# Performance work log

Measured on AMD Instinct MI355X. Metric: run time of the kernel, lower is better.

Reference implementation:

```python
import jax, jax.numpy as jnp
import numpy as np

N_NODES = 100000
N_EDGES = 1600000
N_FEAT = 128
HIDDEN = 16
EMBED = 128
N_GRAPHS = 64


def setup_inputs() -> dict:
    key = jax.random.key(0)
    ks = jax.random.split(key, 6)
    x = jax.random.normal(ks[0], (N_NODES, N_FEAT), dtype=jnp.float32)
    edge_index = jax.random.randint(ks[1], (2, N_EDGES), 0, N_NODES, dtype=jnp.int32)
    batch = jnp.sort(jax.random.randint(ks[2], (N_NODES,), 0, N_GRAPHS, dtype=jnp.int32))
    W1 = jax.random.normal(ks[3], (N_FEAT, HIDDEN), dtype=jnp.float32) * (1.0 / np.sqrt(N_FEAT))
    b1 = jnp.zeros((HIDDEN,), dtype=jnp.float32)
    W2 = jax.random.normal(ks[4], (HIDDEN, EMBED), dtype=jnp.float32) * (1.0 / np.sqrt(HIDDEN))
    b2 = jnp.zeros((EMBED,), dtype=jnp.float32)
    return {"x": x, "edge_index": edge_index, "batch": batch,
            "W1": W1, "b1": b1, "W2": W2, "b2": b2}


def _gcn_conv(x, W, b, src, dst, dinv):
    # x' = D^{-1/2} (A + I) D^{-1/2} (x W) + b ; (src, dst) already include self-loops
    h = x @ W                                   # [N, out]
    norm = dinv[src] * dinv[dst]                # [E']
    msg = h[src] * norm[:, None]                # gather + scale
    out = jax.ops.segment_sum(msg, dst, num_segments=x.shape[0])  # scatter-add
    return out + b


def reference(x, edge_index, batch, W1, b1, W2, b2):
    n = x.shape[0]
    loop = jnp.arange(n, dtype=edge_index.dtype)
    src = jnp.concatenate([edge_index[0], loop])  # add self-loops
    dst = jnp.concatenate([edge_index[1], loop])
    deg = jax.ops.segment_sum(jnp.ones_like(dst, dtype=x.dtype), dst, num_segments=n)
    dinv = jnp.where(deg > 0, jax.lax.rsqrt(deg), 0.0)

    h = _gcn_conv(x, W1, b1, src, dst, dinv)
    h = jax.nn.relu(h)
    # dropout(p=0.2) is identity in eval mode
    h = _gcn_conv(h, W2, b2, src, dst, dinv)

    # mean pooling over graphs in the batch
    sums = jax.ops.segment_sum(h, batch, num_segments=N_GRAPHS)          # [G, EMBED]
    cnt = jax.ops.segment_sum(jnp.ones((n,), dtype=h.dtype), batch, num_segments=N_GRAPHS)
    return sums / jnp.maximum(cnt, 1.0)[:, None]
```

## Files before the change

### kernel.cpp

```cpp
#include <hip/hip_runtime.h>

#define HIDDEN 16
#define N_FEAT 128
#define EMBED 128
#define N_GRAPHS 64
#define BSH 8
#define MAXB 512

__global__ void k_hist(const int* __restrict__ dst, int n_edges, int nbuck,
                       int* __restrict__ ghist) {
    __shared__ int h[MAXB];
    for (int i = threadIdx.x; i < MAXB; i += blockDim.x) h[i] = 0;
    __syncthreads();
    int base = blockIdx.x * blockDim.x * 4;
    for (int j = 0; j < 4; j++) {
        int e = base + j * blockDim.x + threadIdx.x;
        if (e < n_edges) atomicAdd(&h[dst[e] >> BSH], 1);
    }
    __syncthreads();
    for (int b = threadIdx.x; b < nbuck; b += blockDim.x)
        if (h[b]) atomicAdd(&ghist[b], h[b]);
}

__global__ void k_scan(const int* __restrict__ ghist, int nbuck,
                       int* __restrict__ gbase, int* __restrict__ gfill) {
    __shared__ int s[MAXB];
    int t = threadIdx.x;
    s[t] = (t < nbuck) ? ghist[t] : 0;
    __syncthreads();
    for (int st = 1; st < MAXB; st <<= 1) {
        int v = (t >= st) ? s[t - st] : 0;
        __syncthreads();
        s[t] += v;
        __syncthreads();
    }
    if (t < nbuck) {
        int excl = s[t] - ghist[t];
        gbase[t] = excl;
        gfill[t] = excl;
    }
}

__global__ void __launch_bounds__(1024)
k_part(const int* __restrict__ src, const int* __restrict__ dst,
       int n_edges, int nbuck, int* __restrict__ gfill, uint2* __restrict__ ebuf) {
    __shared__ int hcnt[MAXB];
    __shared__ int hexcl[MAXB];
    __shared__ int hrank[MAXB];
    __shared__ int hbase[MAXB];
    __shared__ uint2 stage[4096];
    int tid = threadIdx.x;
    for (int i = tid; i < MAXB; i += 1024) { hcnt[i] = 0; hrank[i] = 0; }
    __syncthreads();
    int base = blockIdx.x * 4096;
    int cnt = min(4096, n_edges - base);
    int s_[4], d_[4];
#pragma unroll
    for (int j = 0; j < 4; j++) {
        int k = j * 1024 + tid;
        if (k < cnt) {
            s_[j] = src[base + k]; d_[j] = dst[base + k];
            atomicAdd(&hcnt[d_[j] >> BSH], 1);
        }
    }
    __syncthreads();
    if (tid < MAXB) hexcl[tid] = hcnt[tid];
    __syncthreads();
    for (int st = 1; st < MAXB; st <<= 1) {
        int v = 0;
        if (tid < MAXB && tid >= st) v = hexcl[tid - st];
        __syncthreads();
        if (tid < MAXB) hexcl[tid] += v;
        __syncthreads();
    }
    if (tid < nbuck && hcnt[tid] > 0)
        hbase[tid] = atomicAdd(&gfill[tid], hcnt[tid]);
    __syncthreads();
#pragma unroll
    for (int j = 0; j < 4; j++) {
        int k = j * 1024 + tid;
        if (k < cnt) {
            int b = d_[j] >> BSH;
            int r = atomicAdd(&hrank[b], 1);
            stage[hexcl[b] - hcnt[b] + r] = make_uint2((unsigned)s_[j], (unsigned)d_[j]);
        }
    }
    __syncthreads();
    for (int t = tid; t < cnt; t += 1024) {
        uint2 e = stage[t];
        int b = (int)(e.y >> BSH);
        ebuf[hbase[b] + (t - (hexcl[b] - hcnt[b]))] = e;
    }
}

__global__ void __launch_bounds__(1024)
k_csr(const uint2* __restrict__ ebuf, const int* __restrict__ gbase,
      const int* __restrict__ ghist, int n,
      int* __restrict__ deg, int* __restrict__ rowp, int* __restrict__ col) {
    __shared__ int nh[256], nexcl[256], nrank[256];
    int b = blockIdx.x;
    int tid = threadIdx.x;
    int seg0 = gbase[b];
    int cnt = ghist[b];
    int nb0 = b << BSH;
    if (tid < 256) { nh[tid] = 0; nrank[tid] = 0; }
    __syncthreads();
    for (int t = tid; t < cnt; t += 1024)
        atomicAdd(&nh[ebuf[seg0 + t].y - nb0], 1);
    __syncthreads();
    if (tid < 256) nexcl[tid] = nh[tid];
    __syncthreads();
    for (int st = 1; st < 256; st <<= 1) {
        int v = 0;
        if (tid < 256 && tid >= st) v = nexcl[tid - st];
        __syncthreads();
        if (tid < 256) nexcl[tid] += v;
        __syncthreads();
    }
    if (tid < 256) {
        int node = nb0 + tid;
        if (node < n) {
            deg[node]  = nh[tid];
            rowp[node] = seg0 + nexcl[tid] - nh[tid];
        }
    }
    __syncthreads();
    for (int t = tid; t < cnt; t += 1024) {
        uint2 e = ebuf[seg0 + t];
        int ln = (int)e.y - nb0;
        int r = atomicAdd(&nrank[ln], 1);
        col[seg0 + (nexcl[ln] - nh[ln]) + r] = (int)e.x;
    }
}

__global__ void k_gemm1(const float* __restrict__ x, const float* __restrict__ W1,
                        const int* __restrict__ deg, float* __restrict__ dinv,
                        float* __restrict__ Hs, int n) {
    __shared__ float Ws[N_FEAT * HIDDEN];
    int tid = threadIdx.x;
    {
        const float4* w4 = (const float4*)W1;
        float4* s4 = (float4*)Ws;
        s4[tid * 2]     = w4[tid * 2];
        s4[tid * 2 + 1] = w4[tid * 2 + 1];
    }
    __syncthreads();
    int i = blockIdx.x * blockDim.x + tid;
    if (i >= n) return;

    float acc[HIDDEN];
#pragma unroll
    for (int o = 0; o < HIDDEN; o++) acc[o] = 0.f;

    const float4* xr = (const float4*)(x + (size_t)i * N_FEAT);
#pragma unroll 8
    for (int k4 = 0; k4 < N_FEAT / 4; k4++) {
        float4 xv = xr[k4];
        const float* w0 = &Ws[(k4 * 4 + 0) * HIDDEN];
        const float* w1 = &Ws[(k4 * 4 + 1) * HIDDEN];
        const float* w2 = &Ws[(k4 * 4 + 2) * HIDDEN];
        const float* w3 = &Ws[(k4 * 4 + 3) * HIDDEN];
#pragma unroll
        for (int o = 0; o < HIDDEN; o++)
            acc[o] += xv.x * w0[o] + xv.y * w1[o] + xv.z * w2[o] + xv.w * w3[o];
    }
    float di = rsqrtf((float)deg[i] + 1.0f);
    dinv[i] = di;
    float4* hout = (float4*)(Hs + (size_t)i * HIDDEN);
#pragma unroll
    for (int q = 0; q < 4; q++) {
        float4 v;
        v.x = acc[q * 4 + 0] * di; v.y = acc[q * 4 + 1] * di;
        v.z = acc[q * 4 + 2] * di; v.w = acc[q * 4 + 3] * di;
        hout[q] = v;
    }
}

template <int LAYER>
__global__ void k_pull(const float* __restrict__ V, const int* __restrict__ rowptr,
                       const int* __restrict__ deg, const int* __restrict__ col,
                       const float* __restrict__ dinv, const float* __restrict__ b1,
                       float* __restrict__ out, int n) {
    int wid = (blockIdx.x * blockDim.x + threadIdx.x) >> 6;
    int lane = threadIdx.x & 63;
    if (wid >= n) return;
    int f  = lane & 15;
    int es = lane >> 4;
    int start = rowptr[wid];
    int dg = deg[wid];
    float acc = 0.f;
    for (int j = es; j < dg; j += 4) {
        int s = col[start + j];
        acc += V[(size_t)s * HIDDEN + f];
    }
    acc += __shfl_xor(acc, 16, 64);
    acc += __shfl_xor(acc, 32, 64);
    if (lane < 16) {
        float tot = acc + V[(size_t)wid * HIDDEN + f];
        float di = dinv[wid];
        float r;
        if (LAYER == 1) r = fmaxf(di * tot + b1[f], 0.f) * di;
        else            r = di * tot;
        out[(size_t)wid * HIDDEN + f] = r;
    }
}

__global__ void k_pool(const float* __restrict__ R, const int* __restrict__ batch,
                       float* __restrict__ S, float* __restrict__ cnt, int n) {
    __shared__ float ls[8][HIDDEN];
    __shared__ float lc[8];
    int tid = threadIdx.x;
    if (tid < 8) lc[tid] = 0.f;
    if (tid < 8 * HIDDEN) ((float*)ls)[tid] = 0.f;
    __syncthreads();

    int i0 = blockIdx.x * blockDim.x;
    int g0 = batch[i0 < n ? i0 : (n - 1)];
    int i = i0 + tid;
    if (i < n) {
        int g = batch[i];
        const float* r = R + (size_t)i * HIDDEN;
        int off = g - g0;
        if (off >= 0 && off < 8) {
#pragma unroll
            for (int o = 0; o < HIDDEN; o++) atomicAdd(&ls[off][o], r[o]);
            atomicAdd(&lc[off], 1.f);
        } else {
#pragma unroll
            for (int o = 0; o < HIDDEN; o++) atomicAdd(&S[(size_t)g * HIDDEN + o], r[o]);
            atomicAdd(&cnt[g], 1.f);
        }
    }
    __syncthreads();
    if (tid < 8 * HIDDEN) {
        int bb = tid >> 4, o = tid & 15;
        int g = g0 + bb;
        float v = ls[bb][o];
        if (v != 0.f && g < N_GRAPHS) atomicAdd(&S[(size_t)g * HIDDEN + o], v);
    }
    if (tid < 8) {
        int g = g0 + tid;
        float c = lc[tid];
        if (c != 0.f && g < N_GRAPHS) atomicAdd(&cnt[g], c);
    }
}

__global__ void k_out(const float* __restrict__ S, const float* __restrict__ cnt,
                      const float* __restrict__ W2, const float* __restrict__ b2,
                      float* __restrict__ out) {
    int g = blockIdx.x;
    int e = threadIdx.x;
    float c = cnt[g];
    float acc = 0.f;
#pragma unroll
    for (int k = 0; k < HIDDEN; k++) acc += S[g * HIDDEN + k] * W2[k * EMBED + e];
    out[g * EMBED + e] = (c > 0.f) ? (acc / c + b2[e]) : 0.f;
}

extern "C" void kernel_launch(void* const* d_in, const int* in_sizes, int n_in,
                              void* d_out, int out_size, void* d_ws, size_t ws_size,
                              hipStream_t stream) {
    const float* x     = (const float*)d_in[0];
    const int*   ei    = (const int*)  d_in[1];
    const int*   batch = (const int*)  d_in[2];
    const float* W1    = (const float*)d_in[3];
    const float* b1    = (const float*)d_in[4];
    const float* W2    = (const float*)d_in[5];
    const float* b2    = (const float*)d_in[6];
    float* out = (float*)d_out;

    const int n       = in_sizes[2];
    const int n_edges = in_sizes[1] / 2;
    const int* srcp = ei;
    const int* dstp = ei + n_edges;
    const int nbuck = (n + 255) >> BSH;

    float* ws    = (float*)d_ws;
    float* Hs    = ws;
    float* Q     = Hs + (size_t)n * HIDDEN;
    float* dinv  = Q + (size_t)n * HIDDEN;
    int*   deg   = (int*)(dinv + n);
    int*   rowp  = deg + n;
    int*   col   = rowp + n;
    int*   ghist = col + n_edges;
    int*   gbase = ghist + MAXB;
    int*   gfill = gbase + MAXB;
    float* S     = (float*)(gfill + MAXB);
    float* cnt   = S + N_GRAPHS * HIDDEN;
    uint2* ebuf  = (uint2*)Hs;

    hipMemsetAsync(ghist, 0, MAXB * sizeof(int), stream);
    hipMemsetAsync(S, 0, (N_GRAPHS * HIDDEN + N_GRAPHS) * sizeof(float), stream);

    const int pb4k = (n_edges + 4095) / 4096;
    k_hist<<<pb4k, 1024, 0, stream>>>(dstp, n_edges, nbuck, ghist);
    k_scan<<<1, MAXB, 0, stream>>>(ghist, nbuck, gbase, gfill);
    k_part<<<pb4k, 1024, 0, stream>>>(srcp, dstp, n_edges, nbuck, gfill, ebuf);
    k_csr <<<nbuck, 1024, 0, stream>>>(ebuf, gbase, ghist, n, deg, rowp, col);

    const int nb = (n + 255) / 256;
    k_gemm1<<<nb, 256, 0, stream>>>(x, W1, deg, dinv, Hs, n);

    const int pullb = (n * 64 + 255) / 256;
    k_pull<1><<<pullb, 256, 0, stream>>>(Hs, rowp, deg, col, dinv, b1, Q, n);
    k_pull<2><<<pullb, 256, 0, stream>>>(Q,  rowp, deg, col, dinv, b1, Hs, n);

    k_pool<<<nb, 256, 0, stream>>>(Hs, batch, S, cnt, n);
    k_out <<<N_GRAPHS, EMBED, 0, stream>>>(S, cnt, W2, b2, out);
}
```

Baseline: 279.0 us.

## Replace CSR build with bucketed aggregation, bf16 features, fused layer-2 pooling

Drops the per-node CSR construction and instead aggregates directly over the destination-bucketed edge buffer, packing the source index and local destination into a single 32-bit word. Hidden features are stored as bf16 pairs to halve gather traffic. The second-layer aggregation is fused with mean pooling, so edge messages are accumulated straight into per-graph sums without materialising layer-2 node outputs. This trades the CSR column build and one full node-feature pass for shared-memory atomics and reduced precision. The 8-bit local-index packing also assumes source indices fit in 24 bits.

```diff
diff --git a/kernel.cpp b/kernel.cpp
--- a/kernel.cpp
+++ b/kernel.cpp
@@ -7,18 +7,31 @@
 #define BSH 8
 #define MAXB 512
 
-__global__ void k_hist(const int* __restrict__ dst, int n_edges, int nbuck,
-                       int* __restrict__ ghist) {
+typedef unsigned int uint;
+
+__device__ inline uint pk2(float a, float b) {
+    uint ua = __float_as_uint(a), ub = __float_as_uint(b);
+    ua = (ua + 0x7FFFu + ((ua >> 16) & 1u)) >> 16;
+    ub = (ub + 0x7FFFu + ((ub >> 16) & 1u)) & 0xFFFF0000u;
+    return ua | ub;
+}
+__device__ inline float2 upk2(uint w) {
+    return make_float2(__uint_as_float(w << 16), __uint_as_float(w & 0xFFFF0000u));
+}
+
+__global__ void __launch_bounds__(1024)
+k_hist(const int* __restrict__ dst, int n_edges, int nbuck, int* __restrict__ ghist) {
     __shared__ int h[MAXB];
-    for (int i = threadIdx.x; i < MAXB; i += blockDim.x) h[i] = 0;
-    __syncthreads();
-    int base = blockIdx.x * blockDim.x * 4;
+    for (int i = threadIdx.x; i < MAXB; i += 1024) h[i] = 0;
+    __syncthreads();
+    int base = blockIdx.x * 4096;
+#pragma unroll
     for (int j = 0; j < 4; j++) {
-        int e = base + j * blockDim.x + threadIdx.x;
+        int e = base + j * 1024 + threadIdx.x;
         if (e < n_edges) atomicAdd(&h[dst[e] >> BSH], 1);
     }
     __syncthreads();
-    for (int b = threadIdx.x; b < nbuck; b += blockDim.x)
+    for (int b = threadIdx.x; b < nbuck; b += 1024)
         if (h[b]) atomicAdd(&ghist[b], h[b]);
 }
 
@@ -43,7 +56,7 @@
 
 __global__ void __launch_bounds__(1024)
 k_part(const int* __restrict__ src, const int* __restrict__ dst,
-       int n_edges, int nbuck, int* __restrict__ gfill, uint2* __restrict__ ebuf) {
+       int n_edges, int nbuck, int* __restrict__ gfill, uint* __restrict__ ebuf) {
     __shared__ int hcnt[MAXB];
     __shared__ int hexcl[MAXB];
     __shared__ int hrank[MAXB];
@@ -82,60 +95,35 @@
         if (k < cnt) {
             int b = d_[j] >> BSH;
             int r = atomicAdd(&hrank[b], 1);
-            stage[hexcl[b] - hcnt[b] + r] = make_uint2((unsigned)s_[j], (unsigned)d_[j]);
+            stage[hexcl[b] - hcnt[b] + r] = make_uint2((uint)s_[j], (uint)d_[j]);
         }
     }
     __syncthreads();
     for (int t = tid; t < cnt; t += 1024) {
         uint2 e = stage[t];
         int b = (int)(e.y >> BSH);
-        ebuf[hbase[b] + (t - (hexcl[b] - hcnt[b]))] = e;
-    }
-}
-
-__global__ void __launch_bounds__(1024)
-k_csr(const uint2* __restrict__ ebuf, const int* __restrict__ gbase,
-      const int* __restrict__ ghist, int n,
-      int* __restrict__ deg, int* __restrict__ rowp, int* __restrict__ col) {
-    __shared__ int nh[256], nexcl[256], nrank[256];
-    int b = blockIdx.x;
-    int tid = threadIdx.x;
-    int seg0 = gbase[b];
-    int cnt = ghist[b];
-    int nb0 = b << BSH;
-    if (tid < 256) { nh[tid] = 0; nrank[tid] = 0; }
-    __syncthreads();
+        ebuf[hbase[b] + (t - (hexcl[b] - hcnt[b]))] = (e.x << 8) | (e.y & 255u);
+    }
+}
+
+__global__ void __launch_bounds__(1024)
+k_deg2(const uint* __restrict__ ebuf, const int* __restrict__ gbase,
+       const int* __restrict__ ghist, int n, int* __restrict__ deg) {
+    __shared__ int nh[256];
+    int tid = threadIdx.x;
+    if (tid < 256) nh[tid] = 0;
+    __syncthreads();
+    int seg0 = gbase[blockIdx.x], cnt = ghist[blockIdx.x];
     for (int t = tid; t < cnt; t += 1024)
-        atomicAdd(&nh[ebuf[seg0 + t].y - nb0], 1);
-    __syncthreads();
-    if (tid < 256) nexcl[tid] = nh[tid];
-    __syncthreads();
-    for (int st = 1; st < 256; st <<= 1) {
-        int v = 0;
-        if (tid < 256 && tid >= st) v = nexcl[tid - st];
-        __syncthreads();
-        if (tid < 256) nexcl[tid] += v;
-        __syncthreads();
-    }
-    if (tid < 256) {
-        int node = nb0 + tid;
-        if (node < n) {
-            deg[node]  = nh[tid];
-            rowp[node] = seg0 + nexcl[tid] - nh[tid];
-        }
-    }
-    __syncthreads();
-    for (int t = tid; t < cnt; t += 1024) {
-        uint2 e = ebuf[seg0 + t];
-        int ln = (int)e.y - nb0;
-        int r = atomicAdd(&nrank[ln], 1);
-        col[seg0 + (nexcl[ln] - nh[ln]) + r] = (int)e.x;
-    }
+        atomicAdd(&nh[ebuf[seg0 + t] & 255u], 1);
+    __syncthreads();
+    int node = (blockIdx.x << BSH) + tid;
+    if (tid < 256 && node < n) deg[node] = nh[tid];
 }
 
 __global__ void k_gemm1(const float* __restrict__ x, const float* __restrict__ W1,
                         const int* __restrict__ deg, float* __restrict__ dinv,
-                        float* __restrict__ Hs, int n) {
+                        uint* __restrict__ Hs2, int n) {
     __shared__ float Ws[N_FEAT * HIDDEN];
     int tid = threadIdx.x;
     {
@@ -166,64 +154,83 @@
     }
     float di = rsqrtf((float)deg[i] + 1.0f);
     dinv[i] = di;
-    float4* hout = (float4*)(Hs + (size_t)i * HIDDEN);
-#pragma unroll
-    for (int q = 0; q < 4; q++) {
-        float4 v;
-        v.x = acc[q * 4 + 0] * di; v.y = acc[q * 4 + 1] * di;
-        v.z = acc[q * 4 + 2] * di; v.w = acc[q * 4 + 3] * di;
-        hout[q] = v;
-    }
-}
-
-template <int LAYER>
-__global__ void k_pull(const float* __restrict__ V, const int* __restrict__ rowptr,
-                       const int* __restrict__ deg, const int* __restrict__ col,
-                       const float* __restrict__ dinv, const float* __restrict__ b1,
-                       float* __restrict__ out, int n) {
-    int wid = (blockIdx.x * blockDim.x + threadIdx.x) >> 6;
-    int lane = threadIdx.x & 63;
-    if (wid >= n) return;
-    int f  = lane & 15;
-    int es = lane >> 4;
-    int start = rowptr[wid];
-    int dg = deg[wid];
-    float acc = 0.f;
-    for (int j = es; j < dg; j += 4) {
-        int s = col[start + j];
-        acc += V[(size_t)s * HIDDEN + f];
-    }
-    acc += __shfl_xor(acc, 16, 64);
-    acc += __shfl_xor(acc, 32, 64);
-    if (lane < 16) {
-        float tot = acc + V[(size_t)wid * HIDDEN + f];
-        float di = dinv[wid];
-        float r;
-        if (LAYER == 1) r = fmaxf(di * tot + b1[f], 0.f) * di;
-        else            r = di * tot;
-        out[(size_t)wid * HIDDEN + f] = r;
-    }
-}
-
-__global__ void k_pool(const float* __restrict__ R, const int* __restrict__ batch,
-                       float* __restrict__ S, float* __restrict__ cnt, int n) {
-    __shared__ float ls[8][HIDDEN];
+    uint o8[8];
+#pragma unroll
+    for (int j = 0; j < 8; j++) o8[j] = pk2(acc[2 * j] * di, acc[2 * j + 1] * di);
+    uint4* hp = (uint4*)(Hs2 + (size_t)i * 8);
+    hp[0] = make_uint4(o8[0], o8[1], o8[2], o8[3]);
+    hp[1] = make_uint4(o8[4], o8[5], o8[6], o8[7]);
+}
+
+__global__ void __launch_bounds__(1024)
+k_agg1(const uint* __restrict__ ebuf, const int* __restrict__ gbase,
+       const int* __restrict__ ghist, const uint* __restrict__ Hs2,
+       const float* __restrict__ dinv, const float* __restrict__ b1,
+       uint* __restrict__ Q2, int n) {
+    __shared__ float Qa[256 * 17];
+    __shared__ float b1s[HIDDEN];
+    int tid = threadIdx.x;
+    for (int i = tid; i < 256 * 17; i += 1024) Qa[i] = 0.f;
+    if (tid < HIDDEN) b1s[tid] = b1[tid];
+    __syncthreads();
+    int seg0 = gbase[blockIdx.x], cnt = ghist[blockIdx.x];
+    int gid = tid >> 3, fp = tid & 7;
+    for (int t = gid; t < cnt; t += 128) {
+        uint e = ebuf[seg0 + t];
+        int s = (int)(e >> 8), ln = (int)(e & 255u);
+        float2 v = upk2(Hs2[(size_t)s * 8 + fp]);
+        atomicAdd(&Qa[ln * 17 + 2 * fp],     v.x);
+        atomicAdd(&Qa[ln * 17 + 2 * fp + 1], v.y);
+    }
+    __syncthreads();
+    int node = (blockIdx.x << BSH) + tid;
+    if (tid < 256 && node < n) {
+        float di = dinv[node];
+        float q[HIDDEN];
+#pragma unroll
+        for (int j = 0; j < 8; j++) {
+            float2 h = upk2(Hs2[(size_t)node * 8 + j]);
+            q[2 * j]     = Qa[tid * 17 + 2 * j]     + h.x;
+            q[2 * j + 1] = Qa[tid * 17 + 2 * j + 1] + h.y;
+        }
+        uint o8[8];
+#pragma unroll
+        for (int j = 0; j < 8; j++) {
+            float a = fmaxf(di * q[2 * j]     + b1s[2 * j],     0.f) * di;
+            float b = fmaxf(di * q[2 * j + 1] + b1s[2 * j + 1], 0.f) * di;
+            o8[j] = pk2(a, b);
+        }
+        uint4* qp = (uint4*)(Q2 + (size_t)node * 8);
+        qp[0] = make_uint4(o8[0], o8[1], o8[2], o8[3]);
+        qp[1] = make_uint4(o8[4], o8[5], o8[6], o8[7]);
+    }
+}
+
+__global__ void k_selfpool(const uint* __restrict__ Q2, const int* __restrict__ batch,
+                           const float* __restrict__ dinv,
+                           float* __restrict__ S, float* __restrict__ cnt, int n) {
+    __shared__ float ls[8 * HIDDEN];
     __shared__ float lc[8];
     int tid = threadIdx.x;
     if (tid < 8) lc[tid] = 0.f;
-    if (tid < 8 * HIDDEN) ((float*)ls)[tid] = 0.f;
-    __syncthreads();
-
-    int i0 = blockIdx.x * blockDim.x;
+    if (tid < 8 * HIDDEN) ls[tid] = 0.f;
+    __syncthreads();
+    int i0 = blockIdx.x * 256;
     int g0 = batch[i0 < n ? i0 : (n - 1)];
     int i = i0 + tid;
     if (i < n) {
         int g = batch[i];
-        const float* r = R + (size_t)i * HIDDEN;
+        float di = dinv[i];
+        float r[HIDDEN];
+#pragma unroll
+        for (int j = 0; j < 8; j++) {
+            float2 v = upk2(Q2[(size_t)i * 8 + j]);
+            r[2 * j] = di * v.x; r[2 * j + 1] = di * v.y;
+        }
         int off = g - g0;
         if (off >= 0 && off < 8) {
 #pragma unroll
-            for (int o = 0; o < HIDDEN; o++) atomicAdd(&ls[off][o], r[o]);
+            for (int o = 0; o < HIDDEN; o++) atomicAdd(&ls[off * HIDDEN + o], r[o]);
             atomicAdd(&lc[off], 1.f);
         } else {
 #pragma unroll
@@ -233,9 +240,9 @@
     }
     __syncthreads();
     if (tid < 8 * HIDDEN) {
-        int bb = tid >> 4, o = tid & 15;
-        int g = g0 + bb;
-        float v = ls[bb][o];
+        int b = tid >> 4, o = tid & 15;
+        int g = g0 + b;
+        float v = ls[b * HIDDEN + o];
         if (v != 0.f && g < N_GRAPHS) atomicAdd(&S[(size_t)g * HIDDEN + o], v);
     }
     if (tid < 8) {
@@ -243,6 +250,50 @@
         float c = lc[tid];
         if (c != 0.f && g < N_GRAPHS) atomicAdd(&cnt[g], c);
     }
+}
+
+__global__ void __launch_bounds__(1024)
+k_edge2(const uint* __restrict__ ebuf, const int* __restrict__ gbase,
+        const int* __restrict__ ghist, const uint* __restrict__ Q2,
+        const int* __restrict__ batch, const float* __restrict__ dinv,
+        float* __restrict__ S, int n) {
+    __shared__ float Sl[N_GRAPHS * HIDDEN];
+    __shared__ int   batL[256];
+    __shared__ float dinvL[256];
+    int tid = threadIdx.x;
+    Sl[tid] = 0.f;
+    if (tid < 256) {
+        int node = (blockIdx.x << BSH) + tid;
+        batL[tid]  = (node < n) ? batch[node] : 0;
+        dinvL[tid] = (node < n) ? dinv[node]  : 0.f;
+    }
+    __syncthreads();
+    int seg0 = gbase[blockIdx.x], cnt = ghist[blockIdx.x];
+    int gid = tid >> 3, fp = tid & 7;
+    int gc = -1;
+    float ax = 0.f, ay = 0.f;
+    for (int t = gid; t < cnt; t += 128) {
+        uint e = ebuf[seg0 + t];
+        int s = (int)(e >> 8), ln = (int)(e & 255u);
+        int g = batL[ln];
+        if (g != gc) {
+            if (gc >= 0) {
+                atomicAdd(&Sl[gc * HIDDEN + 2 * fp],     ax);
+                atomicAdd(&Sl[gc * HIDDEN + 2 * fp + 1], ay);
+            }
+            gc = g; ax = 0.f; ay = 0.f;
+        }
+        float di = dinvL[ln];
+        float2 v = upk2(Q2[(size_t)s * 8 + fp]);
+        ax += di * v.x; ay += di * v.y;
+    }
+    if (gc >= 0) {
+        atomicAdd(&Sl[gc * HIDDEN + 2 * fp],     ax);
+        atomicAdd(&Sl[gc * HIDDEN + 2 * fp + 1], ay);
+    }
+    __syncthreads();
+    float v = Sl[tid];
+    if (v != 0.f) atomicAdd(&S[tid], v);
 }
 
 __global__ void k_out(const float* __restrict__ S, const float* __restrict__ cnt,
@@ -275,36 +326,30 @@
     const int* dstp = ei + n_edges;
     const int nbuck = (n + 255) >> BSH;
 
-    float* ws    = (float*)d_ws;
-    float* Hs    = ws;
-    float* Q     = Hs + (size_t)n * HIDDEN;
-    float* dinv  = Q + (size_t)n * HIDDEN;
+    uint*  Hs2   = (uint*)d_ws;
+    uint*  Q2    = Hs2 + (size_t)n * 8;
+    float* dinv  = (float*)(Q2 + (size_t)n * 8);
     int*   deg   = (int*)(dinv + n);
-    int*   rowp  = deg + n;
-    int*   col   = rowp + n;
-    int*   ghist = col + n_edges;
+    uint*  ebuf  = (uint*)(deg + n);
+    int*   ghist = (int*)(ebuf + n_edges);
     int*   gbase = ghist + MAXB;
     int*   gfill = gbase + MAXB;
     float* S     = (float*)(gfill + MAXB);
     float* cnt   = S + N_GRAPHS * HIDDEN;
-    uint2* ebuf  = (uint2*)Hs;
 
     hipMemsetAsync(ghist, 0, MAXB * sizeof(int), stream);
     hipMemsetAsync(S, 0, (N_GRAPHS * HIDDEN + N_GRAPHS) * sizeof(float), stream);
 
     const int pb4k = (n_edges + 4095) / 4096;
-    k_hist<<<pb4k, 1024, 0, stream>>>(dstp, n_edges, nbuck, ghist);
-    k_scan<<<1, MAXB, 0, stream>>>(ghist, nbuck, gbase, gfill);
-    k_part<<<pb4k, 1024, 0, stream>>>(srcp, dstp, n_edges, nbuck, gfill, ebuf);
-    k_csr <<<nbuck, 1024, 0, stream>>>(ebuf, gbase, ghist, n, deg, rowp, col);
+    k_hist <<<pb4k, 1024, 0, stream>>>(dstp, n_edges, nbuck, ghist);
+    k_scan <<<1, MAXB, 0, stream>>>(ghist, nbuck, gbase, gfill);
+    k_part <<<pb4k, 1024, 0, stream>>>(srcp, dstp, n_edges, nbuck, gfill, ebuf);
+    k_deg2 <<<nbuck, 1024, 0, stream>>>(ebuf, gbase, ghist, n, deg);
 
     const int nb = (n + 255) / 256;
-    k_gemm1<<<nb, 256, 0, stream>>>(x, W1, deg, dinv, Hs, n);
-
-    const int pullb = (n * 64 + 255) / 256;
-    k_pull<1><<<pullb, 256, 0, stream>>>(Hs, rowp, deg, col, dinv, b1, Q, n);
-    k_pull<2><<<pullb, 256, 0, stream>>>(Q,  rowp, deg, col, dinv, b1, Hs, n);
-
-    k_pool<<<nb, 256, 0, stream>>>(Hs, batch, S, cnt, n);
-    k_out <<<N_GRAPHS, EMBED, 0, stream>>>(S, cnt, W2, b2, out);
-}
+    k_gemm1<<<nb, 256, 0, stream>>>(x, W1, deg, dinv, Hs2, n);
+    k_agg1 <<<nbuck, 1024, 0, stream>>>(ebuf, gbase, ghist, Hs2, dinv, b1, Q2, n);
+    k_selfpool<<<nb, 256, 0, stream>>>(Q2, batch, dinv, S, cnt, n);
+    k_edge2<<<nbuck, 1024, 0, stream>>>(ebuf, gbase, ghist, Q2, batch, dinv, S, n);
+    k_out  <<<N_GRAPHS, EMBED, 0, stream>>>(S, cnt, W2, b2, out);
+}
```

New measurement: 425.3 us. 1.52x slower.

## Store node features as bf16 pairs and pack edges into single words

Applied to the files above, without the earlier changes.

Node features Hs and Q are now stored as packed bf16 pairs, which halves the bytes read in the random gathers of both pull kernels. Each wavefront now spreads 8 edges across 8 lanes per feature pair. Edges in the partition buffer are packed as (src<<8 | dst&255), halving partition traffic, and the bucket index is recovered by a binary search over the shared-memory prefix sums. The cost is bf16 rounding error in the intermediate features, plus a log-time search per staged edge.

```diff
diff --git a/kernel.cpp b/kernel.cpp
--- a/kernel.cpp
+++ b/kernel.cpp
@@ -7,18 +7,31 @@
 #define BSH 8
 #define MAXB 512
 
-__global__ void k_hist(const int* __restrict__ dst, int n_edges, int nbuck,
-                       int* __restrict__ ghist) {
+typedef unsigned int uint;
+
+__device__ inline uint pk2(float a, float b) {
+    uint ua = __float_as_uint(a), ub = __float_as_uint(b);
+    ua = (ua + 0x7FFFu + ((ua >> 16) & 1u)) >> 16;
+    ub = (ub + 0x7FFFu + ((ub >> 16) & 1u)) & 0xFFFF0000u;
+    return ua | ub;
+}
+__device__ inline float2 upk2(uint w) {
+    return make_float2(__uint_as_float(w << 16), __uint_as_float(w & 0xFFFF0000u));
+}
+
+__global__ void __launch_bounds__(1024)
+k_hist(const int* __restrict__ dst, int n_edges, int nbuck, int* __restrict__ ghist) {
     __shared__ int h[MAXB];
-    for (int i = threadIdx.x; i < MAXB; i += blockDim.x) h[i] = 0;
-    __syncthreads();
-    int base = blockIdx.x * blockDim.x * 4;
+    for (int i = threadIdx.x; i < MAXB; i += 1024) h[i] = 0;
+    __syncthreads();
+    int base = blockIdx.x * 4096;
+#pragma unroll
     for (int j = 0; j < 4; j++) {
-        int e = base + j * blockDim.x + threadIdx.x;
+        int e = base + j * 1024 + threadIdx.x;
         if (e < n_edges) atomicAdd(&h[dst[e] >> BSH], 1);
     }
     __syncthreads();
-    for (int b = threadIdx.x; b < nbuck; b += blockDim.x)
+    for (int b = threadIdx.x; b < nbuck; b += 1024)
         if (h[b]) atomicAdd(&ghist[b], h[b]);
 }
 
@@ -43,12 +56,12 @@
 
 __global__ void __launch_bounds__(1024)
 k_part(const int* __restrict__ src, const int* __restrict__ dst,
-       int n_edges, int nbuck, int* __restrict__ gfill, uint2* __restrict__ ebuf) {
+       int n_edges, int nbuck, int* __restrict__ gfill, uint* __restrict__ ebuf) {
     __shared__ int hcnt[MAXB];
     __shared__ int hexcl[MAXB];
     __shared__ int hrank[MAXB];
     __shared__ int hbase[MAXB];
-    __shared__ uint2 stage[4096];
+    __shared__ uint stage[4096];
     int tid = threadIdx.x;
     for (int i = tid; i < MAXB; i += 1024) { hcnt[i] = 0; hrank[i] = 0; }
     __syncthreads();
@@ -82,19 +95,24 @@
         if (k < cnt) {
             int b = d_[j] >> BSH;
             int r = atomicAdd(&hrank[b], 1);
-            stage[hexcl[b] - hcnt[b] + r] = make_uint2((unsigned)s_[j], (unsigned)d_[j]);
+            stage[hexcl[b] - hcnt[b] + r] = ((uint)s_[j] << 8) | ((uint)d_[j] & 255u);
         }
     }
     __syncthreads();
     for (int t = tid; t < cnt; t += 1024) {
-        uint2 e = stage[t];
-        int b = (int)(e.y >> BSH);
+        uint e = stage[t];
+        int lo = 0, hi = MAXB - 1;
+        while (lo < hi) {
+            int mid = (lo + hi) >> 1;
+            if (t < hexcl[mid]) hi = mid; else lo = mid + 1;
+        }
+        int b = lo;
         ebuf[hbase[b] + (t - (hexcl[b] - hcnt[b]))] = e;
     }
 }
 
 __global__ void __launch_bounds__(1024)
-k_csr(const uint2* __restrict__ ebuf, const int* __restrict__ gbase,
+k_csr(const uint* __restrict__ ebuf, const int* __restrict__ gbase,
       const int* __restrict__ ghist, int n,
       int* __restrict__ deg, int* __restrict__ rowp, int* __restrict__ col) {
     __shared__ int nh[256], nexcl[256], nrank[256];
@@ -106,7 +124,7 @@
     if (tid < 256) { nh[tid] = 0; nrank[tid] = 0; }
     __syncthreads();
     for (int t = tid; t < cnt; t += 1024)
-        atomicAdd(&nh[ebuf[seg0 + t].y - nb0], 1);
+        atomicAdd(&nh[ebuf[seg0 + t] & 255u], 1);
     __syncthreads();
     if (tid < 256) nexcl[tid] = nh[tid];
     __syncthreads();
@@ -126,16 +144,16 @@
     }
     __syncthreads();
     for (int t = tid; t < cnt; t += 1024) {
-        uint2 e = ebuf[seg0 + t];
-        int ln = (int)e.y - nb0;
+        uint e = ebuf[seg0 + t];
+        int ln = (int)(e & 255u);
         int r = atomicAdd(&nrank[ln], 1);
-        col[seg0 + (nexcl[ln] - nh[ln]) + r] = (int)e.x;
+        col[seg0 + (nexcl[ln] - nh[ln]) + r] = (int)(e >> 8);
     }
 }
 
 __global__ void k_gemm1(const float* __restrict__ x, const float* __restrict__ W1,
                         const int* __restrict__ deg, float* __restrict__ dinv,
-                        float* __restrict__ Hs, int n) {
+                        uint* __restrict__ Hs2, int n) {
     __shared__ float Ws[N_FEAT * HIDDEN];
     int tid = threadIdx.x;
     {
@@ -166,55 +184,59 @@
     }
     float di = rsqrtf((float)deg[i] + 1.0f);
     dinv[i] = di;
-    float4* hout = (float4*)(Hs + (size_t)i * HIDDEN);
-#pragma unroll
-    for (int q = 0; q < 4; q++) {
-        float4 v;
-        v.x = acc[q * 4 + 0] * di; v.y = acc[q * 4 + 1] * di;
-        v.z = acc[q * 4 + 2] * di; v.w = acc[q * 4 + 3] * di;
-        hout[q] = v;
-    }
+    uint o8[8];
+#pragma unroll
+    for (int j = 0; j < 8; j++) o8[j] = pk2(acc[2 * j] * di, acc[2 * j + 1] * di);
+    uint4* hp = (uint4*)(Hs2 + (size_t)i * 8);
+    hp[0] = make_uint4(o8[0], o8[1], o8[2], o8[3]);
+    hp[1] = make_uint4(o8[4], o8[5], o8[6], o8[7]);
 }
 
 template <int LAYER>
-__global__ void k_pull(const float* __restrict__ V, const int* __restrict__ rowptr,
+__global__ void k_pull(const uint* __restrict__ V2, const int* __restrict__ rowptr,
                        const int* __restrict__ deg, const int* __restrict__ col,
                        const float* __restrict__ dinv, const float* __restrict__ b1,
-                       float* __restrict__ out, int n) {
+                       uint* __restrict__ Q2, float2* __restrict__ R2, int n) {
     int wid = (blockIdx.x * blockDim.x + threadIdx.x) >> 6;
     int lane = threadIdx.x & 63;
     if (wid >= n) return;
-    int f  = lane & 15;
-    int es = lane >> 4;
+    int f  = lane & 7;
+    int es = lane >> 3;
     int start = rowptr[wid];
     int dg = deg[wid];
-    float acc = 0.f;
-    for (int j = es; j < dg; j += 4) {
+    float ax = 0.f, ay = 0.f;
+    for (int j = es; j < dg; j += 8) {
         int s = col[start + j];
-        acc += V[(size_t)s * HIDDEN + f];
-    }
-    acc += __shfl_xor(acc, 16, 64);
-    acc += __shfl_xor(acc, 32, 64);
-    if (lane < 16) {
-        float tot = acc + V[(size_t)wid * HIDDEN + f];
+        float2 v = upk2(V2[(size_t)s * 8 + f]);
+        ax += v.x; ay += v.y;
+    }
+    ax += __shfl_xor(ax, 8, 64);  ay += __shfl_xor(ay, 8, 64);
+    ax += __shfl_xor(ax, 16, 64); ay += __shfl_xor(ay, 16, 64);
+    ax += __shfl_xor(ax, 32, 64); ay += __shfl_xor(ay, 32, 64);
+    if (lane < 8) {
+        float2 h = upk2(V2[(size_t)wid * 8 + f]);
+        float tx = ax + h.x, ty = ay + h.y;
         float di = dinv[wid];
-        float r;
-        if (LAYER == 1) r = fmaxf(di * tot + b1[f], 0.f) * di;
-        else            r = di * tot;
-        out[(size_t)wid * HIDDEN + f] = r;
+        if (LAYER == 1) {
+            float qa = fmaxf(di * tx + b1[2 * f],     0.f) * di;
+            float qb = fmaxf(di * ty + b1[2 * f + 1], 0.f) * di;
+            Q2[(size_t)wid * 8 + f] = pk2(qa, qb);
+        } else {
+            R2[(size_t)wid * 8 + f] = make_float2(di * tx, di * ty);
+        }
     }
 }
 
 __global__ void k_pool(const float* __restrict__ R, const int* __restrict__ batch,
                        float* __restrict__ S, float* __restrict__ cnt, int n) {
-    __shared__ float ls[8][HIDDEN];
+    __shared__ float ls[8 * HIDDEN];
     __shared__ float lc[8];
     int tid = threadIdx.x;
     if (tid < 8) lc[tid] = 0.f;
-    if (tid < 8 * HIDDEN) ((float*)ls)[tid] = 0.f;
-    __syncthreads();
-
-    int i0 = blockIdx.x * blockDim.x;
+    if (tid < 8 * HIDDEN) ls[tid] = 0.f;
+    __syncthreads();
+
+    int i0 = blockIdx.x * 256;
     int g0 = batch[i0 < n ? i0 : (n - 1)];
     int i = i0 + tid;
     if (i < n) {
@@ -223,7 +245,7 @@
         int off = g - g0;
         if (off >= 0 && off < 8) {
 #pragma unroll
-            for (int o = 0; o < HIDDEN; o++) atomicAdd(&ls[off][o], r[o]);
+            for (int o = 0; o < HIDDEN; o++) atomicAdd(&ls[off * HIDDEN + o], r[o]);
             atomicAdd(&lc[off], 1.f);
         } else {
 #pragma unroll
@@ -233,9 +255,9 @@
     }
     __syncthreads();
     if (tid < 8 * HIDDEN) {
-        int bb = tid >> 4, o = tid & 15;
-        int g = g0 + bb;
-        float v = ls[bb][o];
+        int b = tid >> 4, o = tid & 15;
+        int g = g0 + b;
+        float v = ls[b * HIDDEN + o];
         if (v != 0.f && g < N_GRAPHS) atomicAdd(&S[(size_t)g * HIDDEN + o], v);
     }
     if (tid < 8) {
@@ -275,36 +297,36 @@
     const int* dstp = ei + n_edges;
     const int nbuck = (n + 255) >> BSH;
 
-    float* ws    = (float*)d_ws;
-    float* Hs    = ws;
-    float* Q     = Hs + (size_t)n * HIDDEN;
-    float* dinv  = Q + (size_t)n * HIDDEN;
+    uint*  Hs2   = (uint*)d_ws;
+    uint*  Q2    = Hs2 + (size_t)n * 8;
+    float* dinv  = (float*)(Q2 + (size_t)n * 8);
     int*   deg   = (int*)(dinv + n);
     int*   rowp  = deg + n;
     int*   col   = rowp + n;
-    int*   ghist = col + n_edges;
+    uint*  ebuf  = (uint*)(col + n_edges);
+    int*   ghist = (int*)(ebuf + n_edges);
     int*   gbase = ghist + MAXB;
     int*   gfill = gbase + MAXB;
     float* S     = (float*)(gfill + MAXB);
     float* cnt   = S + N_GRAPHS * HIDDEN;
-    uint2* ebuf  = (uint2*)Hs;
+    float* R     = (float*)ebuf;
 
     hipMemsetAsync(ghist, 0, MAXB * sizeof(int), stream);
     hipMemsetAsync(S, 0, (N_GRAPHS * HIDDEN + N_GRAPHS) * sizeof(float), stream);
 
     const int pb4k = (n_edges + 4095) / 4096;
-    k_hist<<<pb4k, 1024, 0, stream>>>(dstp, n_edges, nbuck, ghist);
-    k_scan<<<1, MAXB, 0, stream>>>(ghist, nbuck, gbase, gfill);
-    k_part<<<pb4k, 1024, 0, stream>>>(srcp, dstp, n_edges, nbuck, gfill, ebuf);
-    k_csr <<<nbuck, 1024, 0, stream>>>(ebuf, gbase, ghist, n, deg, rowp, col);
+    k_hist <<<pb4k, 1024, 0, stream>>>(dstp, n_edges, nbuck, ghist);
+    k_scan <<<1, MAXB, 0, stream>>>(ghist, nbuck, gbase, gfill);
+    k_part <<<pb4k, 1024, 0, stream>>>(srcp, dstp, n_edges, nbuck, gfill, ebuf);
+    k_csr  <<<nbuck, 1024, 0, stream>>>(ebuf, gbase, ghist, n, deg, rowp, col);
 
     const int nb = (n + 255) / 256;
-    k_gemm1<<<nb, 256, 0, stream>>>(x, W1, deg, dinv, Hs, n);
+    k_gemm1<<<nb, 256, 0, stream>>>(x, W1, deg, dinv, Hs2, n);
 
     const int pullb = (n * 64 + 255) / 256;
-    k_pull<1><<<pullb, 256, 0, stream>>>(Hs, rowp, deg, col, dinv, b1, Q, n);
-    k_pull<2><<<pullb, 256, 0, stream>>>(Q,  rowp, deg, col, dinv, b1, Hs, n);
-
-    k_pool<<<nb, 256, 0, stream>>>(Hs, batch, S, cnt, n);
-    k_out <<<N_GRAPHS, EMBED, 0, stream>>>(S, cnt, W2, b2, out);
-}
+    k_pull<1><<<pullb, 256, 0, stream>>>(Hs2, rowp, deg, col, dinv, b1, Q2, (float2*)R, n);
+    k_pull<2><<<pullb, 256, 0, stream>>>(Q2,  rowp, deg, col, dinv, b1, Hs2, (float2*)R, n);
+
+    k_pool <<<nb, 256, 0, stream>>>(R, batch, S, cnt, n);
+    k_out  <<<N_GRAPHS, EMBED, 0, stream>>>(S, cnt, W2, b2, out);
+}
```

Result: faster. 255.1 us (-8.6%).
